# Optimization experiments

Measured on AMD Instinct MI355X. Metric: run time of the kernel, lower is better.

The kernel has to match this reference:

```python
import jax, jax.numpy as jnp
import numpy as np

B, S, D, H = 4, 2048, 1024, 16
HD = D // H  # head dim = 64


def setup_inputs() -> dict:
    key = jax.random.key(0)
    ks = jax.random.split(key, 11)
    std = 1.0 / np.sqrt(D)
    return {
        "query": jax.random.normal(ks[0], (B, S, D), jnp.float32),
        "key": jax.random.normal(ks[1], (B, S, D), jnp.float32),
        "value": jax.random.normal(ks[2], (B, S, D), jnp.float32),
        "Wq": jax.random.normal(ks[3], (D, D), jnp.float32) * std,
        "bq": jnp.zeros((D,), jnp.float32),
        "Wk": jax.random.normal(ks[4], (D, D), jnp.float32) * std,
        "bk": jnp.zeros((D,), jnp.float32),
        "Wv": jax.random.normal(ks[5], (D, D), jnp.float32) * std,
        "bv": jnp.zeros((D,), jnp.float32),
        "Wo": jax.random.normal(ks[6], (D, D), jnp.float32) * std,
        "bo": jnp.zeros((D,), jnp.float32),
    }


def reference(query, key, value, Wq, bq, Wk, bk, Wv, bv, Wo, bo):
    scale = jnp.sqrt(jnp.float32(D))  # NOTE: module scales by sqrt(hid_dim), not sqrt(head_dim)
    # nn.Linear: x @ W.T + b
    def split_heads(x):
        return x.reshape(B, -1, H, HD).transpose(0, 2, 1, 3)  # [B,H,S,HD]
    Q = split_heads(query @ Wq.T + bq)
    K = split_heads(key @ Wk.T + bk)
    V = split_heads(value @ Wv.T + bv)
    energy = jnp.einsum("bhqd,bhkd->bhqk", Q, K) / scale  # [B,H,S,S]
    attention = jax.nn.softmax(energy, axis=-1)  # dropout is identity in eval / p=0
    X = jnp.einsum("bhqk,bhkd->bhqd", attention, V)  # [B,H,S,HD]
    X = X.transpose(0, 2, 1, 3).reshape(B, -1, D)  # [B,S,D]
    return X @ Wo.T + bo
```

## Files before the change

### kernel.cpp

```cpp
#include <hip/hip_runtime.h>
#include <stdint.h>

#define DEVI __device__ __forceinline__

typedef __attribute__((ext_vector_type(8))) __bf16 bf16x8;
typedef __attribute__((ext_vector_type(4))) __bf16 bf16x4;
typedef __attribute__((ext_vector_type(4))) float f32x4;
typedef __attribute__((ext_vector_type(4))) unsigned short u16x4;
typedef __attribute__((ext_vector_type(4))) unsigned int u32x4;
typedef unsigned short u16;

constexpr int Bn = 4, Sn = 2048, Dn = 1024, Hn = 16;
constexpr int Mn = Bn * Sn;
constexpr float QSCALE = 1.4426950408889634f / 32.0f;
constexpr float SSHIFT = -16.0f;

DEVI u16 f2bf(float f) {
  uint32_t u = __builtin_bit_cast(uint32_t, f);
  u += 0x7fffu + ((u >> 16) & 1u);
  return (u16)(u >> 16);
}

typedef __attribute__((address_space(1))) void gvoid;
typedef __attribute__((address_space(3))) void lvoid;
DEVI void gload_lds16(const void* g, void* l) {
  __builtin_amdgcn_global_load_lds((gvoid*)(uintptr_t)g,
                                   (lvoid*)(uint32_t)(uintptr_t)l, 16, 0, 0);
}

DEVI f32x4 mfma16(bf16x8 a, bf16x8 b, f32x4 c) {
  return __builtin_amdgcn_mfma_f32_16x16x32_bf16(a, b, c, 0, 0, 0);
}

struct CastArgs {
  const float* src[4];
  u16* dst[4];
  int n[4];
};

__global__ __launch_bounds__(256) void cast_kernel(CastArgs a) {
  const int seg = blockIdx.y;
  const float* __restrict__ src = a.src[seg];
  u16* __restrict__ dst = a.dst[seg];
  const int n = a.n[seg];
  const int stride = gridDim.x * 256 * 4;
  for (int i = (blockIdx.x * 256 + threadIdx.x) * 4; i < n; i += stride) {
    const float4 v = *reinterpret_cast<const float4*>(src + i);
    u16x4 p;
    p[0] = f2bf(v.x); p[1] = f2bf(v.y); p[2] = f2bf(v.z); p[3] = f2bf(v.w);
    *reinterpret_cast<u16x4*>(dst + i) = p;
  }
}

struct QKVArgs {
  const float *Aq, *Ak, *Av;
  const u16 *Wq, *Wk, *Wv;
  const float *bq, *bk, *bv;
  u16 *Qh, *Kh, *Vt;
};

__global__ __launch_bounds__(512, 4)
void qkv_gemm(QKVArgs a) {
  __shared__ __align__(16) float Asf[3][128 * 32];
  __shared__ __align__(16) u16 Bs[3][128 * 32];

  const int raw = blockIdx.x;
  const int swz = (raw & 7) * 192 + (raw >> 3);
  const int which = swz >> 9;
  const int bid = swz & 511;
  const float* __restrict__ A = which == 0 ? a.Aq : which == 1 ? a.Ak : a.Av;
  const u16* __restrict__ Bt  = which == 0 ? a.Wq : which == 1 ? a.Wk : a.Wv;
  const float* __restrict__ bias = which == 0 ? a.bq : which == 1 ? a.bk : a.bv;

  const int mt = bid >> 3, nt = bid & 7;
  const int m0 = mt * 128, n0 = nt * 128;

  const int tid = threadIdx.x, lane = tid & 63, w = tid >> 6;
  const int wr = w >> 1, wc = w & 1;
  const int c = lane & 15, g = lane >> 4;

  const int arow = tid >> 3;
  const int aus = (tid & 7) ^ (arow & 7);
  const float* aSrc = A + (size_t)(m0 + arow) * 1024 + aus * 4;
  const u16* bSrc = Bt + (size_t)(n0 + arow + 64 * (aus >> 2)) * 1024 + (aus & 3) * 8;
  const int ldsOff = w * 1024;

  const int aB0 = (wr * 32 + c) * 128 + (((g * 2) ^ (c & 7)) << 4);
  const int bB0 = c * 128 + (((wc * 4 + g) ^ (c & 7)) << 4);

  f32x4 acc[2][4] = {};

#define QSTAGE(BUF, KT_)                                                      \
  {                                                                           \
    gload_lds16(aSrc + (KT_), (char*)Asf[BUF] + ldsOff);                      \
    gload_lds16(aSrc + 65536 + (KT_), (char*)Asf[BUF] + 8192 + ldsOff);       \
    gload_lds16(bSrc + (KT_), (char*)Bs[BUF] + ldsOff);                      \
  }

#define QTILE(BUF, SBUF, KT)                                                  \
  {                                                                           \
    asm volatile("s_waitcnt vmcnt(3)" ::: "memory");                          \
    __builtin_amdgcn_sched_barrier(0);                                        \
    __builtin_amdgcn_s_barrier();                                             \
    __builtin_amdgcn_sched_barrier(0);                                        \
    QSTAGE(SBUF, ((KT) + 64) & 1023);                                         \
    bf16x8 bfq[4];                                                            \
    _Pragma("unroll")                                                         \
    for (int ni = 0; ni < 4; ++ni)                                            \
      bfq[ni] = *(const bf16x8*)((const char*)Bs[BUF] + bB0 + ni * 2048);     \
    bf16x8 af[2];                                                             \
    _Pragma("unroll")                                                         \
    for (int mi = 0; mi < 2; ++mi) {                                          \
      const f32x4 alo = *(const f32x4*)((const char*)Asf[BUF] + (aB0 + mi * 2048));        \
      const f32x4 ahi = *(const f32x4*)((const char*)Asf[BUF] + ((aB0 ^ 16) + mi * 2048)); \
      uint32_t w0_, w1_, w2_, w3_;                                            \
      asm("v_cvt_pk_bf16_f32 %0, %1, %2" : "=v"(w0_) : "v"(alo[0]), "v"(alo[1])); \
      asm("v_cvt_pk_bf16_f32 %0, %1, %2" : "=v"(w1_) : "v"(alo[2]), "v"(alo[3])); \
      asm("v_cvt_pk_bf16_f32 %0, %1, %2" : "=v"(w2_) : "v"(ahi[0]), "v"(ahi[1])); \
      asm("v_cvt_pk_bf16_f32 %0, %1, %2" : "=v"(w3_) : "v"(ahi[2]), "v"(ahi[3])); \
      const u32x4 uv_ = {w0_, w1_, w2_, w3_};                                 \
      af[mi] = __builtin_bit_cast(bf16x8, uv_);                               \
    }                                                                         \
    __builtin_amdgcn_s_setprio(1);                                            \
    _Pragma("unroll")                                                         \
    for (int mi = 0; mi < 2; ++mi)                                            \
      _Pragma("unroll")                                                       \
      for (int ni = 0; ni < 4; ++ni)                                          \
        acc[mi][ni] = mfma16(af[mi], bfq[ni], acc[mi][ni]);                   \
    __builtin_amdgcn_s_setprio(0);                                            \
  }

  QSTAGE(0, 0);
  QSTAGE(1, 32);
  for (int kt = 0; kt < 960; kt += 96) {
    QTILE(0, 2, kt);
    QTILE(1, 0, kt + 32);
    QTILE(2, 1, kt + 64);
  }
  QTILE(0, 2, 960);
  QTILE(1, 0, 992);
#undef QTILE
#undef QSTAGE

  #pragma unroll
  for (int mi = 0; mi < 2; ++mi) {
    #pragma unroll
    for (int ni = 0; ni < 4; ++ni) {
      const int n = n0 + wc * 64 + ni * 16 + c;
      const float bv = bias[n];
      const int mb = m0 + wr * 32 + mi * 16 + g * 4;
      const f32x4 v = acc[mi][ni];
      const int h = n >> 6, hd = n & 63;
      if (which == 2) {
        const int b = mb >> 11, s = mb & 2047;
        u16x4 pk;
        #pragma unroll
        for (int j = 0; j < 4; ++j) pk[j] = f2bf(v[j] + bv);
        *(u16x4*)(a.Vt + ((size_t)((b * Hn + h) * 64 + hd)) * Sn + s) = pk;
      } else {
        u16* dst = which == 0 ? a.Qh : a.Kh;
        const float sc = which == 0 ? QSCALE : 1.0f;
        #pragma unroll
        for (int j = 0; j < 4; ++j) {
          const int m = mb + j;
          const int b = m >> 11, s = m & 2047;
          dst[(((size_t)(b * Hn + h) * Sn + s) << 6) + hd] = f2bf((v[j] + bv) * sc);
        }
      }
    }
  }
}

__global__ __launch_bounds__(512, 4)
void gemm_out(const u16* __restrict__ A, const u16* __restrict__ Bt,
              const float* __restrict__ bias, float* __restrict__ out) {
  __shared__ __align__(16) u16 As[3][128 * 32];
  __shared__ __align__(16) u16 Bs[3][256 * 32];

  const int raw = blockIdx.x;
  const int swz = (raw & 7) * 32 + (raw >> 3);
  const int mt = swz >> 2, nt = swz & 3;
  const int m0 = mt * 128, n0 = nt * 256;

  const int tid = threadIdx.x, lane = tid & 63, w = tid >> 6;
  const int wr = w >> 2, wc = w & 3;
  const int c = lane & 15, g = lane >> 4;
  const int arow = tid >> 3;
  const int aus = (tid & 7) ^ (arow & 7);
  const u16* aSrc = A + (size_t)(m0 + arow + 64 * (aus >> 2)) * 1024 + (aus & 3) * 8;
  const u16* bSrc0 = Bt + (size_t)(n0 + arow + 128 * (aus >> 2)) * 1024 + (aus & 3) * 8;
  const u16* bSrc1 = bSrc0 + (size_t)64 * 1024;
  const int ldsOff = w * 1024;
  const int aBr = c * 128 + (((wr * 4 + g) ^ (c & 7)) << 4);
  const int bBr = (wc & 1) * 8192 + c * 128
                  + ((((wc >> 1) * 4 + g) ^ (c & 7)) << 4);

  f32x4 acc[4][4] = {};

#define OSTAGE(BUF, KT_)                                                      \
  {                                                                           \
    gload_lds16(aSrc + (KT_), (char*)As[BUF] + ldsOff);                       \
    gload_lds16(bSrc0 + (KT_), (char*)Bs[BUF] + ldsOff);                      \
    gload_lds16(bSrc1 + (KT_), (char*)Bs[BUF] + 8192 + ldsOff);               \
  }

#define OTILE(BUF, SBUF, KT)                                                  \
  {                                                                           \
    asm volatile("s_waitcnt vmcnt(3)" ::: "memory");                          \
    __builtin_amdgcn_sched_barrier(0);                                        \
    __builtin_amdgcn_s_barrier();                                             \
    __builtin_amdgcn_sched_barrier(0);                                        \
    OSTAGE(SBUF, ((KT) + 64) & 1023);                                         \
    bf16x8 af[4], bfq[4];                                                     \
    _Pragma("unroll")                                                         \
    for (int i = 0; i < 4; ++i)                                               \
      af[i] = *(const bf16x8*)((const char*)As[BUF] + aBr + i * 2048);        \
    _Pragma("unroll")                                                         \
    for (int i = 0; i < 4; ++i)                                               \
      bfq[i] = *(const bf16x8*)((const char*)Bs[BUF] + bBr + i * 2048);       \
    __builtin_amdgcn_s_setprio(1);                                            \
    _Pragma("unroll")                                                         \
    for (int mi = 0; mi < 4; ++mi)                                            \
      _Pragma("unroll")                                                       \
      for (int ni = 0; ni < 4; ++ni)                                          \
        acc[mi][ni] = mfma16(af[mi], bfq[ni], acc[mi][ni]);                   \
    __builtin_amdgcn_s_setprio(0);                                            \
  }

  OSTAGE(0, 0);
  OSTAGE(1, 32);
  for (int kt = 0; kt < 960; kt += 96) {
    OTILE(0, 2, kt);
    OTILE(1, 0, kt + 32);
    OTILE(2, 1, kt + 64);
  }
  OTILE(0, 2, 960);
  OTILE(1, 0, 992);
#undef OTILE
#undef OSTAGE

  #pragma unroll
  for (int mi = 0; mi < 4; ++mi) {
    #pragma unroll
    for (int ni = 0; ni < 4; ++ni) {
      const int n = n0 + wc * 64 + ni * 16 + c;
      const float bv = bias[n];
      const int mb = m0 + wr * 64 + mi * 16 + g * 4;
      const f32x4 v = acc[mi][ni];
      #pragma unroll
      for (int j = 0; j < 4; ++j)
        out[(size_t)(mb + j) * Dn + n] = v[j] + bv;
    }
  }
}

__global__ __launch_bounds__(512, 4)
void flash_attn(const u16* __restrict__ Q, const u16* __restrict__ K,
                const u16* __restrict__ Vt, u16* __restrict__ X) {
  __shared__ __align__(16) u16 Ks[3][4096];
  __shared__ __align__(16) u16 Vs[3][4096];

  const int tid = threadIdx.x, lane = tid & 63, w = tid >> 6;
  const int bid = blockIdx.x;
  const int bh = bid & 63, qt = bid >> 6;
  const int b = bh >> 4, h = bh & 15;
  const int q0 = qt * 128 + w * 16;
  const int c = lane & 15, g = lane >> 4;

  const u16* Qb = Q + (size_t)bh * Sn * 64;
  const u16* Kb = K + (size_t)bh * Sn * 64;
  const u16* Vb = Vt + (size_t)bh * 64 * Sn;

  const int srow = tid >> 3;
  const int scol = (((tid & 7) * 16) ^ ((srow & 7) << 4)) >> 1;
  const int srcK = srow * 64 + scol;
  const int srcV = srow * Sn + scol;
  const int ldsOff = w * 1024;
#define STAGE(BUF, KV_)                                                   \
  {                                                                       \
    gload_lds16(Kb + (size_t)(KV_) * 64 + srcK, (char*)Ks[BUF] + ldsOff); \
    gload_lds16(Vb + (KV_) + srcV, (char*)Vs[BUF] + ldsOff);              \
  }

  const int laneB0 = c * 128 + ((g * 16) ^ ((c & 7) << 4));
  const int laneB1 = c * 128 + ((64 + g * 16) ^ ((c & 7) << 4));

  bf16x8 qf[2];
  #pragma unroll
  for (int ks = 0; ks < 2; ++ks)
    qf[ks] = *(const bf16x8*)(Qb + (size_t)(q0 + c) * 64 + ks * 32 + g * 8);

  bf16x8 ONES;
  #pragma unroll
  for (int e = 0; e < 8; ++e) ONES[e] = (__bf16)1.0f;
  const f32x4 SINITv = {SSHIFT, SSHIFT, SSHIFT, SSHIFT};

  f32x4 o[4] = {};
  f32x4 lacc = {};
  f32x4 scA[4], scB[4];

#define QK_BLOCK(KB, SCT)                                                     \
  {                                                                           \
    bf16x8 kfr[4];                                                            \
    _Pragma("unroll")                                                         \
    for (int kf = 0; kf < 4; ++kf)                                            \
      kfr[kf] = *(const bf16x8*)((const char*)Ks[KB] + laneB0 + kf * 2048);   \
    __builtin_amdgcn_s_setprio(1);                                            \
    _Pragma("unroll")                                                         \
    for (int kf = 0; kf < 4; ++kf)                                            \
      SCT[kf] = mfma16(kfr[kf], qf[0], SINITv);                               \
    __builtin_amdgcn_s_setprio(0);                                            \
    _Pragma("unroll")                                                         \
    for (int kf = 0; kf < 4; ++kf)                                            \
      kfr[kf] = *(const bf16x8*)((const char*)Ks[KB] + laneB1 + kf * 2048);   \
    __builtin_amdgcn_s_setprio(1);                                            \
    _Pragma("unroll")                                                         \
    for (int kf = 0; kf < 4; ++kf)                                            \
      SCT[kf] = mfma16(kfr[kf], qf[1], SCT[kf]);                              \
    __builtin_amdgcn_s_setprio(0);                                            \
  }

#define FIN_BLOCK(VB, SCT)                                                    \
  {                                                                           \
    uint32_t wvv[4][2];                                                       \
    _Pragma("unroll")                                                         \
    for (int kf = 0; kf < 4; ++kf) {                                          \
      const float p0 = __builtin_exp2f(SCT[kf][0]);                           \
      const float p1 = __builtin_exp2f(SCT[kf][1]);                           \
      const float p2 = __builtin_exp2f(SCT[kf][2]);                           \
      const float p3 = __builtin_exp2f(SCT[kf][3]);                           \
      asm("v_cvt_pk_bf16_f32 %0, %1, %2" : "=v"(wvv[kf][0]) : "v"(p0), "v"(p1)); \
      asm("v_cvt_pk_bf16_f32 %0, %1, %2" : "=v"(wvv[kf][1]) : "v"(p2), "v"(p3)); \
    }                                                                         \
    bf16x8 pa[2];                                                             \
    _Pragma("unroll")                                                         \
    for (int ks2 = 0; ks2 < 2; ++ks2) {                                       \
      uint32_t ua = wvv[2 * ks2][0], ub = wvv[2 * ks2][1];                    \
      uint32_t uc = wvv[2 * ks2 + 1][0], ud = wvv[2 * ks2 + 1][1];            \
      asm("v_permlane32_swap_b32 %0, %1" : "+v"(ua), "+v"(uc));               \
      asm("v_permlane32_swap_b32 %0, %1" : "+v"(ub), "+v"(ud));               \
      asm("v_permlane16_swap_b32 %0, %1" : "+v"(ua), "+v"(uc));               \
      asm("v_permlane16_swap_b32 %0, %1" : "+v"(ub), "+v"(ud));               \
      const u32x4 uv = {ua, ub, uc, ud};                                      \
      pa[ks2] = __builtin_bit_cast(bf16x8, uv);                               \
    }                                                                         \
    lacc = mfma16(pa[0], ONES, lacc);                                         \
    lacc = mfma16(pa[1], ONES, lacc);                                         \
    {                                                                         \
      bf16x8 vfr[4];                                                          \
      _Pragma("unroll")                                                       \
      for (int nd = 0; nd < 4; ++nd)                                          \
        vfr[nd] = *(const bf16x8*)((const char*)Vs[VB] + laneB0 + nd * 2048); \
      __builtin_amdgcn_s_setprio(1);                                          \
      _Pragma("unroll")                                                       \
      for (int nd = 0; nd < 4; ++nd)                                          \
        o[nd] = mfma16(pa[0], vfr[nd], o[nd]);                                \
      __builtin_amdgcn_s_setprio(0);                                          \
      _Pragma("unroll")                                                       \
      for (int nd = 0; nd < 4; ++nd)                                          \
        vfr[nd] = *(const bf16x8*)((const char*)Vs[VB] + laneB1 + nd * 2048); \
      __builtin_amdgcn_s_setprio(1);                                          \
      _Pragma("unroll")                                                       \
      for (int nd = 0; nd < 4; ++nd)                                          \
        o[nd] = mfma16(pa[1], vfr[nd], o[nd]);                                \
      __builtin_amdgcn_s_setprio(0);                                          \
    }                                                                         \
  }

#define PIPE(KB, VB, SB, KV, CURT, NXTT)                                      \
  {                                                                           \
    asm volatile("s_waitcnt vmcnt(0)" ::: "memory");                          \
    __builtin_amdgcn_sched_barrier(0);                                        \
    __builtin_amdgcn_s_barrier();                                             \
    __builtin_amdgcn_sched_barrier(0);                                        \
    STAGE(SB, (KV) + 128);                                                    \
    QK_BLOCK(KB, NXTT);                                                       \
    FIN_BLOCK(VB, CURT);                                                      \
  }

  STAGE(0, 0);
  STAGE(1, 64);
  asm volatile("s_waitcnt vmcnt(2)" ::: "memory");
  __builtin_amdgcn_sched_barrier(0);
  __builtin_amdgcn_s_barrier();
  __builtin_amdgcn_sched_barrier(0);
  QK_BLOCK(0, scA);

  for (int kv = 0; kv < 1920; kv += 384) {
    PIPE(1, 0, 2, kv,       scA, scB);
    PIPE(2, 1, 0, kv + 64,  scB, scA);
    PIPE(0, 2, 1, kv + 128, scA, scB);
    PIPE(1, 0, 2, kv + 192, scB, scA);
    PIPE(2, 1, 0, kv + 256, scA, scB);
    PIPE(0, 2, 1, kv + 320, scB, scA);
  }
  asm volatile("s_waitcnt vmcnt(0)" ::: "memory");
  __builtin_amdgcn_sched_barrier(0);
  __builtin_amdgcn_s_barrier();
  __builtin_amdgcn_sched_barrier(0);
  QK_BLOCK(1, scB);
  FIN_BLOCK(0, scA);
  FIN_BLOCK(1, scB);
#undef PIPE
#undef FIN_BLOCK
#undef QK_BLOCK
#undef STAGE

  #pragma unroll
  for (int j = 0; j < 4; ++j) {
    const float rn = 1.0f / lacc[j];
    const int s = q0 + g * 4 + j;
    u16* dst = X + (size_t)(b * Sn + s) * Dn + h * 64 + c;
    #pragma unroll
    for (int nd = 0; nd < 4; ++nd)
      dst[nd * 16] = f2bf(o[nd][j] * rn);
  }
}

extern "C" void kernel_launch(void* const* d_in, const int* in_sizes, int n_in,
                              void* d_out, int out_size, void* d_ws, size_t ws_size,
                              hipStream_t stream) {
  (void)in_sizes; (void)n_in; (void)out_size; (void)ws_size;
  const float* query = (const float*)d_in[0];
  const float* key_  = (const float*)d_in[1];
  const float* value = (const float*)d_in[2];
  const float* Wq = (const float*)d_in[3];
  const float* bq = (const float*)d_in[4];
  const float* Wk = (const float*)d_in[5];
  const float* bk = (const float*)d_in[6];
  const float* Wv = (const float*)d_in[7];
  const float* bv = (const float*)d_in[8];
  const float* Wo = (const float*)d_in[9];
  const float* bo = (const float*)d_in[10];

  char* ws = (char*)d_ws;
  size_t off = 0;
  auto alloc = [&](size_t bytes) {
    void* p = ws + off;
    off += (bytes + 255) & ~(size_t)255;
    return p;
  };
  const size_t actB = (size_t)Mn * Dn * 2;
  const size_t wB = (size_t)Dn * Dn * 2;
  u16* wqb = (u16*)alloc(wB);
  u16* wkb = (u16*)alloc(wB);
  u16* wvb = (u16*)alloc(wB);
  u16* wob = (u16*)alloc(wB);
  u16* Qh = (u16*)alloc(actB);
  u16* Kh = (u16*)alloc(actB);
  u16* Vt = (u16*)alloc(actB);
  u16* Xb = (u16*)alloc(actB);

  CastArgs ca;
  ca.src[0] = Wq; ca.src[1] = Wk; ca.src[2] = Wv; ca.src[3] = Wo;
  ca.dst[0] = wqb; ca.dst[1] = wkb; ca.dst[2] = wvb; ca.dst[3] = wob;
  ca.n[0] = ca.n[1] = ca.n[2] = ca.n[3] = Dn * Dn;
  cast_kernel<<<dim3(512, 4), 256, 0, stream>>>(ca);

  QKVArgs qa;
  qa.Aq = query; qa.Ak = key_; qa.Av = value;
  qa.Wq = wqb; qa.Wk = wkb; qa.Wv = wvb;
  qa.bq = bq; qa.bk = bk; qa.bv = bv;
  qa.Qh = Qh; qa.Kh = Kh; qa.Vt = Vt;
  qkv_gemm<<<dim3(1536), 512, 0, stream>>>(qa);

  flash_attn<<<dim3(Bn * Hn * (Sn / 128)), 512, 0, stream>>>(Qh, Kh, Vt, Xb);
  gemm_out<<<dim3(256), 512, 0, stream>>>(Xb, wob, bo, (float*)d_out);
}
```

Measured before the change: 206.5 us.

## Widen QKV GEMM tile to 128x256 with decoupled A/B LDS buffering

The QKV projection GEMM tile grows from 128x128 to 128x256 per block, so each wave computes 64x64 instead of 32x64 and the grid halves. This cuts redundant fp32 A-tile loads and in-LDS bf16 conversions per output element. A now uses a double buffer and B a triple buffer with separate staging and wait counts. The cost is more accumulator registers and LDS per block (about 80KB), which may reduce occupancy relative to the launch bound of 4.

After: 213.1 us. 1.03x slower.

```diff
diff --git a/kernel.cpp b/kernel.cpp
--- a/kernel.cpp
+++ b/kernel.cpp
@@ -61,58 +61,65 @@
 
 __global__ __launch_bounds__(512, 4)
 void qkv_gemm(QKVArgs a) {
-  __shared__ __align__(16) float Asf[3][128 * 32];
-  __shared__ __align__(16) u16 Bs[3][128 * 32];
+  __shared__ __align__(16) float Asf[2][128 * 32];
+  __shared__ __align__(16) u16 Bs[3][256 * 32];
 
   const int raw = blockIdx.x;
-  const int swz = (raw & 7) * 192 + (raw >> 3);
-  const int which = swz >> 9;
-  const int bid = swz & 511;
+  const int swz = (raw & 7) * 96 + (raw >> 3);
+  const int which = swz >> 8;
+  const int bid = swz & 255;
   const float* __restrict__ A = which == 0 ? a.Aq : which == 1 ? a.Ak : a.Av;
   const u16* __restrict__ Bt  = which == 0 ? a.Wq : which == 1 ? a.Wk : a.Wv;
   const float* __restrict__ bias = which == 0 ? a.bq : which == 1 ? a.bk : a.bv;
 
-  const int mt = bid >> 3, nt = bid & 7;
-  const int m0 = mt * 128, n0 = nt * 128;
+  const int mt = bid >> 2, nt = bid & 3;
+  const int m0 = mt * 128, n0 = nt * 256;
 
   const int tid = threadIdx.x, lane = tid & 63, w = tid >> 6;
-  const int wr = w >> 1, wc = w & 1;
+  const int wr = w >> 2, wc = w & 3;
   const int c = lane & 15, g = lane >> 4;
 
   const int arow = tid >> 3;
   const int aus = (tid & 7) ^ (arow & 7);
   const float* aSrc = A + (size_t)(m0 + arow) * 1024 + aus * 4;
-  const u16* bSrc = Bt + (size_t)(n0 + arow + 64 * (aus >> 2)) * 1024 + (aus & 3) * 8;
+  const u16* bSrc0 = Bt + (size_t)(n0 + arow + 128 * (aus >> 2)) * 1024 + (aus & 3) * 8;
+  const u16* bSrc1 = bSrc0 + (size_t)64 * 1024;
   const int ldsOff = w * 1024;
 
-  const int aB0 = (wr * 32 + c) * 128 + (((g * 2) ^ (c & 7)) << 4);
-  const int bB0 = c * 128 + (((wc * 4 + g) ^ (c & 7)) << 4);
-
-  f32x4 acc[2][4] = {};
-
-#define QSTAGE(BUF, KT_)                                                      \
+  const int aB0 = (wr * 64 + c) * 128 + (((g * 2) ^ (c & 7)) << 4);
+  const int bBr = (wc & 1) * 8192 + c * 128
+                  + ((((wc >> 1) * 4 + g) ^ (c & 7)) << 4);
+
+  f32x4 acc[4][4] = {};
+
+#define QSTAGE_A(BUF, KT_)                                                    \
   {                                                                           \
     gload_lds16(aSrc + (KT_), (char*)Asf[BUF] + ldsOff);                      \
     gload_lds16(aSrc + 65536 + (KT_), (char*)Asf[BUF] + 8192 + ldsOff);       \
-    gload_lds16(bSrc + (KT_), (char*)Bs[BUF] + ldsOff);                      \
-  }
-
-#define QTILE(BUF, SBUF, KT)                                                  \
-  {                                                                           \
-    asm volatile("s_waitcnt vmcnt(3)" ::: "memory");                          \
+  }
+#define QSTAGE_B(BUF, KT_)                                                    \
+  {                                                                           \
+    gload_lds16(bSrc0 + (KT_), (char*)Bs[BUF] + ldsOff);                      \
+    gload_lds16(bSrc1 + (KT_), (char*)Bs[BUF] + 8192 + ldsOff);               \
+  }
+
+#define QTILE(AR, AW, BR, BS, KT)                                             \
+  {                                                                           \
+    asm volatile("s_waitcnt vmcnt(2)" ::: "memory");                          \
     __builtin_amdgcn_sched_barrier(0);                                        \
     __builtin_amdgcn_s_barrier();                                             \
     __builtin_amdgcn_sched_barrier(0);                                        \
-    QSTAGE(SBUF, ((KT) + 64) & 1023);                                         \
+    QSTAGE_A(AW, ((KT) + 32) & 1023);                                         \
+    QSTAGE_B(BS, ((KT) + 64) & 1023);                                         \
     bf16x8 bfq[4];                                                            \
     _Pragma("unroll")                                                         \
     for (int ni = 0; ni < 4; ++ni)                                            \
-      bfq[ni] = *(const bf16x8*)((const char*)Bs[BUF] + bB0 + ni * 2048);     \
-    bf16x8 af[2];                                                             \
-    _Pragma("unroll")                                                         \
-    for (int mi = 0; mi < 2; ++mi) {                                          \
-      const f32x4 alo = *(const f32x4*)((const char*)Asf[BUF] + (aB0 + mi * 2048));        \
-      const f32x4 ahi = *(const f32x4*)((const char*)Asf[BUF] + ((aB0 ^ 16) + mi * 2048)); \
+      bfq[ni] = *(const bf16x8*)((const char*)Bs[BR] + bBr + ni * 2048);      \
+    bf16x8 af[4];                                                             \
+    _Pragma("unroll")                                                         \
+    for (int mi = 0; mi < 4; ++mi) {                                          \
+      const f32x4 alo = *(const f32x4*)((const char*)Asf[AR] + (aB0 + mi * 2048));        \
+      const f32x4 ahi = *(const f32x4*)((const char*)Asf[AR] + ((aB0 ^ 16) + mi * 2048)); \
       uint32_t w0_, w1_, w2_, w3_;                                            \
       asm("v_cvt_pk_bf16_f32 %0, %1, %2" : "=v"(w0_) : "v"(alo[0]), "v"(alo[1])); \
       asm("v_cvt_pk_bf16_f32 %0, %1, %2" : "=v"(w1_) : "v"(alo[2]), "v"(alo[3])); \
@@ -123,32 +130,37 @@
     }                                                                         \
     __builtin_amdgcn_s_setprio(1);                                            \
     _Pragma("unroll")                                                         \
-    for (int mi = 0; mi < 2; ++mi)                                            \
+    for (int mi = 0; mi < 4; ++mi)                                            \
       _Pragma("unroll")                                                       \
       for (int ni = 0; ni < 4; ++ni)                                          \
         acc[mi][ni] = mfma16(af[mi], bfq[ni], acc[mi][ni]);                   \
     __builtin_amdgcn_s_setprio(0);                                            \
   }
 
-  QSTAGE(0, 0);
-  QSTAGE(1, 32);
-  for (int kt = 0; kt < 960; kt += 96) {
-    QTILE(0, 2, kt);
-    QTILE(1, 0, kt + 32);
-    QTILE(2, 1, kt + 64);
-  }
-  QTILE(0, 2, 960);
-  QTILE(1, 0, 992);
+  QSTAGE_A(0, 0);
+  QSTAGE_B(0, 0);
+  QSTAGE_B(1, 32);
+  for (int kt = 0; kt < 960; kt += 192) {
+    QTILE(0, 1, 0, 2, kt);
+    QTILE(1, 0, 1, 0, kt + 32);
+    QTILE(0, 1, 2, 1, kt + 64);
+    QTILE(1, 0, 0, 2, kt + 96);
+    QTILE(0, 1, 1, 0, kt + 128);
+    QTILE(1, 0, 2, 1, kt + 160);
+  }
+  QTILE(0, 1, 0, 2, 960);
+  QTILE(1, 0, 1, 0, 992);
 #undef QTILE
-#undef QSTAGE
+#undef QSTAGE_B
+#undef QSTAGE_A
 
   #pragma unroll
-  for (int mi = 0; mi < 2; ++mi) {
+  for (int mi = 0; mi < 4; ++mi) {
     #pragma unroll
     for (int ni = 0; ni < 4; ++ni) {
       const int n = n0 + wc * 64 + ni * 16 + c;
       const float bv = bias[n];
-      const int mb = m0 + wr * 32 + mi * 16 + g * 4;
+      const int mb = m0 + wr * 64 + mi * 16 + g * 4;
       const f32x4 v = acc[mi][ni];
       const int h = n >> 6, hd = n & 63;
       if (which == 2) {
@@ -462,7 +474,7 @@
   qa.Wq = wqb; qa.Wk = wkb; qa.Wv = wvb;
   qa.bq = bq; qa.bk = bk; qa.bv = bv;
   qa.Qh = Qh; qa.Kh = Kh; qa.Vt = Vt;
-  qkv_gemm<<<dim3(1536), 512, 0, stream>>>(qa);
+  qkv_gemm<<<dim3(768), 512, 0, stream>>>(qa);
 
   flash_attn<<<dim3(Bn * Hn * (Sn / 128)), 512, 0, stream>>>(Qh, Kh, Vt, Xb);
   gemm_out<<<dim3(256), 512, 0, stream>>>(Xb, wob, bo, (float*)d_out);
```
